# Kernel optimization log

Measured on AMD Instinct MI355X. Metric: run time of the kernel, lower is better.

The kernel has to match this reference:

```python
import jax, jax.numpy as jnp
import numpy as np

B = 16384    # batch of game states
HAND = 8     # max_hand_size
A = 30       # max_actions
C = 4        # max cards per action combo
E = 32       # card_embed_dim
HID = 128    # hidden_dim


def _encode_cards(cards, val_emb, suit_emb, type_emb):
    # cards: int array, 0 = padding, 53 = joker (treated as padding for value/suit)
    invalid = (cards == 0) | (cards == 53)
    values = jnp.where(invalid, 0, (cards - 1) % 13 + 1)
    suits = jnp.where(invalid, 0, (cards - 1) // 13 + 1)
    ce = jnp.concatenate([val_emb[values], suit_emb[suits]], axis=-1)  # [..., E]
    ct = jnp.where(values == 11, 1, jnp.where(values == 12, 2, jnp.where(values == 13, 3, 0)))
    te = type_emb[ct]  # [..., 8]
    pad = jnp.zeros(te.shape[:-1] + (E - te.shape[-1],), ce.dtype)
    return ce + jnp.concatenate([te, pad], axis=-1)


def _mha(q, kv, wq, bq, wk, bk, wv, bv, wo, bo, nh, kpm=None):
    b, sq, e = q.shape
    sk = kv.shape[1]
    hd = e // nh
    Q = (q @ wq + bq).reshape(b, sq, nh, hd)
    K = (kv @ wk + bk).reshape(b, sk, nh, hd)
    V = (kv @ wv + bv).reshape(b, sk, nh, hd)
    s = jnp.einsum('bqhd,bkhd->bhqk', Q, K) * (1.0 / np.sqrt(hd))
    if kpm is not None:  # kpm True = valid key
        s = s + jnp.where(kpm[:, None, None, :], 0.0, -1e9)
    a = jax.nn.softmax(s, axis=-1)
    o = jnp.einsum('bhqk,bkhd->bqhd', a, V).reshape(b, sq, e)
    return o @ wo + bo


def _combo_features(cards):
    # cards: [A, C] int, 0 = padding. Vectorized version of _compute_combo_features.
    mask = cards != 0
    combo_size = mask.sum(1).astype(jnp.float32)
    values = jnp.where(mask, (cards - 1) % 13 + 1, 0)
    has_valid = mask.any(1)
    fidx = jnp.argmax(mask, axis=1)
    fv = values[jnp.arange(cards.shape[0]), fidx]  # first valid value per action
    same = jnp.where(mask, values == fv[:, None], True).all(1).astype(jnp.float32)
    vf = values.astype(jnp.float32)
    attack = jnp.where(values == 1, 1.0,
             jnp.where(values == 11, 10.0,
             jnp.where(values == 12, 15.0,
             jnp.where(values == 13, 20.0, vf))))
    total = (attack * mask).sum(1)
    suits = jnp.where(mask, (cards - 1) // 13 + 1, 0)
    uniq = jnp.stack([(suits == s).any(1) for s in (1, 2, 3, 4)], 0).sum(0).astype(jnp.float32)
    ace = ((values == 1) & mask).any(1).astype(jnp.float32)
    valid = ((combo_size <= 4.0) & ((same > 0) | (ace > 0))).astype(jnp.float32)
    feats = jnp.stack([combo_size, same, total, uniq, ace, valid], axis=1)  # [A, 6]
    return jnp.where(has_valid[:, None], feats, 0.0), has_valid


def _forward(hand_cards, enemy_card, hand_size, game_state, discard_pile_cards,
             action_card_indices, num_valid_actions,
             val_emb, suit_emb, type_emb,
             ce_w1, ce_b1, ce_w2, ce_b2,
             ha_wq, ha_bq, ha_wk, ha_bk, ha_wv, ha_bv, ha_wo, ha_bo,
             he_wq, he_bq, he_wk, he_bk, he_wv, he_bv, he_wo, he_bo,
             se_w1, se_b1, se_w2, se_b2,
             atc_w1, atc_b1, atc_w2, atc_b2,
             as_w1, as_b1, as_w2, as_b2, as_w3, as_b3,
             cx_w1, cx_b1, cx_w2, cx_b2, cx_w3, cx_b3):
    relu = jax.nn.relu
    hand_emb = _encode_cards(hand_cards, val_emb, suit_emb, type_emb)            # [B, HAND, E]
    enemy_emb = _encode_cards(enemy_card[:, None], val_emb, suit_emb, type_emb)  # [B, 1, E]
    hand_mask = hand_cards != 0
    attended = _mha(hand_emb, hand_emb, ha_wq, ha_bq, ha_wk, ha_bk, ha_wv, ha_bv, ha_wo, ha_bo, 8, kpm=hand_mask)
    ctx_he = _mha(attended, enemy_emb, he_wq, he_bq, he_wk, he_bk, he_wv, he_bv, he_wo, he_bo, 4)
    lengths = jnp.maximum(hand_size.astype(jnp.float32), 1.0)[:, None]
    hand_ctx = ctx_he.sum(1) / lengths                                           # [B, E]

    # strategic features (batched per game state)
    hvals = jnp.where(hand_cards == 0, 0, (hand_cards - 1) % 13 + 1)
    hsz = hand_size.astype(jnp.float32)
    aces = (hvals == 1).sum(1).astype(jnp.float32)
    faces = ((hvals >= 11) & (hvals <= 13)).sum(1).astype(jnp.float32)
    low = ((hvals >= 2) & (hvals <= 6)).sum(1).astype(jnp.float32)
    hsuits = jnp.where(hand_cards == 0, 0, (hand_cards - 1) // 13 + 1)
    scnt = [(hsuits == s).sum(1).astype(jnp.float32) for s in (1, 2, 3, 4)]
    hvr = faces / (hsz + 1e-8)
    sdiv = jnp.stack([(hsuits == s).any(1) for s in (1, 2, 3, 4)], 0).sum(0).astype(jnp.float32) / 4.0
    strat = jnp.stack([hsz, aces, faces, low, scnt[0], scnt[1], scnt[2], scnt[3], hvr, sdiv], axis=1)
    strat_in = jnp.concatenate([game_state, strat], axis=1)                      # [B, 20]
    strat_ctx = relu(strat_in @ se_w1 + se_b1) @ se_w2 + se_b2                   # [B, 32]

    combined = jnp.concatenate([hand_ctx, enemy_emb[:, 0], strat_ctx, discard_pile_cards], axis=1)  # [B, 150]
    h = relu(combined @ cx_w1 + cx_b1)
    h = relu(h @ cx_w2 + cx_b2)
    ctx = h @ cx_w3 + cx_b3                                                      # [B, HID]
    type_probs = jax.nn.softmax(relu(ctx @ atc_w1 + atc_b1) @ atc_w2 + atc_b2, axis=-1)  # [B, 4]

    feats, has_valid = _combo_features(action_card_indices)                      # [A, 6], [A]
    emb = _encode_cards(action_card_indices, val_emb, suit_emb, type_emb)        # [A, C, E]
    m = (action_card_indices != 0).astype(emb.dtype)[..., None]
    cnt = jnp.maximum(m.sum(1), 1.0)
    act_emb = (emb * m).sum(1) / cnt                                             # masked mean over real cards
    act_emb = jnp.where(has_valid[:, None], act_emb, 0.0)
    combo_enc = relu(feats @ ce_w1 + ce_b1) @ ce_w2 + ce_b2                      # [A, 16]

    Bn = ctx.shape[0]
    af = jnp.concatenate([
        jnp.broadcast_to(ctx[:, None, :], (Bn, A, HID)),
        jnp.broadcast_to(act_emb[None], (Bn, A, E)),
        jnp.broadcast_to(combo_enc[None], (Bn, A, 16)),
    ], axis=-1)                                                                  # [B, A, 176]
    s = relu(af @ as_w1 + as_b1)
    s = relu(s @ as_w2 + as_b2)
    score = (s @ as_w3 + as_b3)[..., 0]                                          # [B, A]

    strength = feats[:, 2] / 20.0                                                # [A]
    bonus_valid = type_probs[:, 0:1] * strength[None, :] + type_probs[:, 1:2] * (1.0 - strength[None, :])
    bonus_empty = jnp.broadcast_to(type_probs[:, 3:4] * 2.0, (Bn, A))
    bonus = jnp.where(has_valid[None, :], bonus_valid, bonus_empty)
    return score + bonus                                                          # [B, A]


def setup_inputs() -> dict:
    key = jax.random.key(0)
    ki = iter(jax.random.split(key, 64))
    def nrm(shape, s):
        return (s * jax.random.normal(next(ki), shape)).astype(jnp.float32)
    def lin(i, o, s=0.08):
        return nrm((i, o), s), nrm((o,), 0.02)
    d = {}
    hc = jax.random.randint(next(ki), (B, HAND), 0, 53)
    d['hand_cards'] = hc.at[:, 0].set(jax.random.randint(next(ki), (B,), 1, 53))  # at least one valid card per hand
    d['enemy_card'] = jax.random.randint(next(ki), (B,), 1, 53)
    d['hand_size'] = jax.random.randint(next(ki), (B,), 1, 9)
    d['game_state'] = nrm((B, 10), 1.0)
    d['discard_pile_cards'] = jax.random.uniform(next(ki), (B, 54), dtype=jnp.float32)
    d['action_card_indices'] = jax.random.randint(next(ki), (A, C), 1, 53)
    d['num_valid_actions'] = A
    d['val_emb'] = nrm((14, 16), 0.1).at[0].set(0.0)   # padding_idx=0
    d['suit_emb'] = nrm((5, 16), 0.1).at[0].set(0.0)   # padding_idx=0
    d['type_emb'] = nrm((4, 8), 0.1)
    d['ce_w1'], d['ce_b1'] = lin(6, 32)
    d['ce_w2'], d['ce_b2'] = lin(32, 16)
    for p in ('ha', 'he'):
        for t in ('q', 'k', 'v', 'o'):
            d[p + '_w' + t], d[p + '_b' + t] = lin(E, E)
    d['se_w1'], d['se_b1'] = lin(20, 64)
    d['se_w2'], d['se_b2'] = lin(64, 32)
    d['atc_w1'], d['atc_b1'] = lin(HID, 64)
    d['atc_w2'], d['atc_b2'] = lin(64, 4)
    d['as_w1'], d['as_b1'] = lin(HID + E + 16, 64)
    d['as_w2'], d['as_b2'] = lin(64, 32)
    d['as_w3'], d['as_b3'] = lin(32, 1)
    d['cx_w1'], d['cx_b1'] = lin(2 * E + 32 + 54, HID)
    d['cx_w2'], d['cx_b2'] = lin(HID, HID)
    d['cx_w3'], d['cx_b3'] = lin(HID, HID)
    return d


def reference(hand_cards, enemy_card, hand_size, game_state, discard_pile_cards,
              action_card_indices, num_valid_actions,
              val_emb, suit_emb, type_emb,
              ce_w1, ce_b1, ce_w2, ce_b2,
              ha_wq, ha_bq, ha_wk, ha_bk, ha_wv, ha_bv, ha_wo, ha_bo,
              he_wq, he_bq, he_wk, he_bk, he_wv, he_bv, he_wo, he_bo,
              se_w1, se_b1, se_w2, se_b2,
              atc_w1, atc_b1, atc_w2, atc_b2,
              as_w1, as_b1, as_w2, as_b2, as_w3, as_b3,
              cx_w1, cx_b1, cx_w2, cx_b2, cx_w3, cx_b3):
    return _forward(hand_cards, enemy_card, hand_size, game_state, discard_pile_cards,
                    action_card_indices, num_valid_actions,
                    val_emb, suit_emb, type_emb,
                    ce_w1, ce_b1, ce_w2, ce_b2,
                    ha_wq, ha_bq, ha_wk, ha_bk, ha_wv, ha_bv, ha_wo, ha_bo,
                    he_wq, he_bq, he_wk, he_bk, he_wv, he_bv, he_wo, he_bo,
                    se_w1, se_b1, se_w2, se_b2,
                    atc_w1, atc_b1, atc_w2, atc_b2,
                    as_w1, as_b1, as_w2, as_b2, as_w3, as_b3,
                    cx_w1, cx_b1, cx_w2, cx_b2, cx_w3, cx_b3)
```

## Files before the change

### kernel.cpp

```cpp
#include <hip/hip_runtime.h>
#include <math.h>


__device__ __forceinline__ void encode_card32(int c,
                                              const float* __restrict__ val_emb,
                                              const float* __restrict__ suit_emb,
                                              const float* __restrict__ type_emb,
                                              float* e) {
  bool inv = (c == 0) || (c == 53);
  int v = inv ? 0 : ((c - 1) % 13 + 1);
  int s = inv ? 0 : ((c - 1) / 13 + 1);
  int ct = (v == 11) ? 1 : (v == 12) ? 2 : (v == 13) ? 3 : 0;
#pragma unroll
  for (int i = 0; i < 16; ++i) e[i] = val_emb[v * 16 + i];
#pragma unroll
  for (int i = 0; i < 16; ++i) e[16 + i] = suit_emb[s * 16 + i];
#pragma unroll
  for (int i = 0; i < 8; ++i) e[i] += type_emb[ct * 8 + i];
}

__global__ __launch_bounds__(64) void action_kernel(
    const int* __restrict__ acards,
    const float* __restrict__ val_emb, const float* __restrict__ suit_emb,
    const float* __restrict__ type_emb,
    const float* __restrict__ ce_w1, const float* __restrict__ ce_b1,
    const float* __restrict__ ce_w2, const float* __restrict__ ce_b2,
    const float* __restrict__ as_w1, const float* __restrict__ as_b1,
    float* __restrict__ ws) {
  __shared__ float sAct[30][32];
  __shared__ float sCombo[30][16];
  const int tid = threadIdx.x;

  if (tid < 30) {
    int c[4];
#pragma unroll
    for (int i = 0; i < 4; ++i) c[i] = acards[tid * 4 + i];
    bool mask[4]; int vals[4], suits[4]; int csize = 0; bool hasv = false;
#pragma unroll
    for (int i = 0; i < 4; ++i) {
      mask[i] = (c[i] != 0);
      if (mask[i]) { csize++; hasv = true; }
      vals[i] = mask[i] ? ((c[i] - 1) % 13 + 1) : 0;
      suits[i] = mask[i] ? ((c[i] - 1) / 13 + 1) : 0;
    }
    int fvv = mask[0] ? vals[0] : mask[1] ? vals[1] : mask[2] ? vals[2]
              : mask[3] ? vals[3] : vals[0];
    bool same = true;
#pragma unroll
    for (int i = 0; i < 4; ++i) if (mask[i] && vals[i] != fvv) same = false;
    float total = 0.f;
#pragma unroll
    for (int i = 0; i < 4; ++i) {
      if (mask[i]) {
        int v = vals[i];
        total += (v == 1) ? 1.f : (v == 11) ? 10.f : (v == 12) ? 15.f
                 : (v == 13) ? 20.f : (float)v;
      }
    }
    float uniq = 0.f;
#pragma unroll
    for (int s = 1; s <= 4; ++s) {
      bool any = false;
#pragma unroll
      for (int i = 0; i < 4; ++i) if (suits[i] == s) any = true;
      uniq += any ? 1.f : 0.f;
    }
    bool ace = false;
#pragma unroll
    for (int i = 0; i < 4; ++i) if (mask[i] && vals[i] == 1) ace = true;
    float f_same = same ? 1.f : 0.f, f_ace = ace ? 1.f : 0.f;
    float valid = (((float)csize <= 4.f) && (f_same > 0.f || f_ace > 0.f)) ? 1.f : 0.f;
    float feats[6] = {(float)csize, f_same, total, uniq, f_ace, valid};
    if (!hasv) { for (int i = 0; i < 6; ++i) feats[i] = 0.f; }
    float emb[32];
#pragma unroll
    for (int i = 0; i < 32; ++i) emb[i] = 0.f;
    float cnt = 0.f;
#pragma unroll
    for (int i = 0; i < 4; ++i) {
      float e[32];
      encode_card32(c[i], val_emb, suit_emb, type_emb, e);
      if (mask[i]) {
#pragma unroll
        for (int j = 0; j < 32; ++j) emb[j] += e[j];
        cnt += 1.f;
      }
    }
    float invc = 1.f / fmaxf(cnt, 1.f);
#pragma unroll
    for (int j = 0; j < 32; ++j) sAct[tid][j] = hasv ? emb[j] * invc : 0.f;
    float t32[32];
#pragma unroll
    for (int j = 0; j < 32; ++j) {
      float acc = ce_b1[j];
#pragma unroll
      for (int k = 0; k < 6; ++k) acc += feats[k] * ce_w1[k * 32 + j];
      t32[j] = fmaxf(acc, 0.f);
    }
#pragma unroll
    for (int j = 0; j < 16; ++j) {
      float acc = ce_b2[j];
#pragma unroll
      for (int k = 0; k < 32; ++k) acc += t32[k] * ce_w2[k * 16 + j];
      sCombo[tid][j] = acc;
    }
    ws[1920 + tid] = total * 0.05f;
    ws[1950 + tid] = hasv ? 1.f : 0.f;
  }
  __syncthreads();
  for (int idx = tid; idx < 1920; idx += 64) {
    int a = idx >> 6, j = idx & 63;
    float acc = as_b1[j];
#pragma unroll
    for (int k = 0; k < 32; ++k) acc += sAct[a][k] * as_w1[(128 + k) * 64 + j];
#pragma unroll
    for (int k = 0; k < 16; ++k) acc += sCombo[a][k] * as_w1[(160 + k) * 64 + j];
    ws[idx] = acc;
  }
}

template <int K, int NJ, bool RELU, bool HASB, bool QIN, bool QOUT>
__device__ __forceinline__ void layerU(
    const float* __restrict__ in, int inColBase, float* __restrict__ outB,
    int outColBase, const float* __restrict__ W, int ldw, int j0,
    const float* __restrict__ bias, int r) {
  float acc[NJ];
#pragma unroll
  for (int j = 0; j < NJ; ++j) acc[j] = HASB ? bias[j0 + j] : 0.f;
  if constexpr (QIN) {
    static_assert(K % 4 == 0, "quad input needs K%4==0");
    const int g0 = inColBase >> 2;
#pragma unroll 8
    for (int g = 0; g < K / 4; ++g) {
      float4 a = *(const float4*)&in[(g0 + g) * 256 + r * 4];
#pragma unroll
      for (int q = 0; q < 4; ++q) {
        float av = (q == 0) ? a.x : (q == 1) ? a.y : (q == 2) ? a.z : a.w;
        const float* wr = W + (size_t)(g * 4 + q) * ldw + j0;
#pragma unroll
        for (int j = 0; j < NJ; ++j) acc[j] += av * wr[j];
      }
    }
  } else {
#pragma unroll 4
    for (int k = 0; k < K; ++k) {
      float a = in[(inColBase + k) * 64 + r];
      const float* wr = W + (size_t)k * ldw + j0;
#pragma unroll
      for (int j = 0; j < NJ; ++j) acc[j] += a * wr[j];
    }
  }
#pragma unroll
  for (int j = 0; j < NJ; ++j) if (RELU) acc[j] = fmaxf(acc[j], 0.f);
  if constexpr (QOUT && (NJ % 4 == 0)) {
    const int c0 = outColBase + j0;
#pragma unroll
    for (int qg = 0; qg < NJ / 4; ++qg) {
      float4 o = make_float4(acc[qg * 4], acc[qg * 4 + 1],
                             acc[qg * 4 + 2], acc[qg * 4 + 3]);
      *(float4*)&outB[((c0 >> 2) + qg) * 256 + r * 4] = o;
    }
  } else {
#pragma unroll
    for (int j = 0; j < NJ; ++j) outB[(outColBase + j0 + j) * 64 + r] = acc[j];
  }
}

__global__ __launch_bounds__(1024) void policy_main(
    const int* __restrict__ hand_cards, const int* __restrict__ enemy_card,
    const int* __restrict__ hand_size, const float* __restrict__ game_state,
    const float* __restrict__ discard,
    const float* __restrict__ val_emb, const float* __restrict__ suit_emb,
    const float* __restrict__ type_emb,
    const float* __restrict__ he_wv, const float* __restrict__ he_bv,
    const float* __restrict__ he_wo, const float* __restrict__ he_bo,
    const float* __restrict__ se_w1, const float* __restrict__ se_b1,
    const float* __restrict__ se_w2, const float* __restrict__ se_b2,
    const float* __restrict__ atc_w1, const float* __restrict__ atc_b1,
    const float* __restrict__ atc_w2, const float* __restrict__ atc_b2,
    const float* __restrict__ as_w1,
    const float* __restrict__ as_w2, const float* __restrict__ as_b2,
    const float* __restrict__ as_w3, const float* __restrict__ as_b3,
    const float* __restrict__ cx_w1, const float* __restrict__ cx_b1,
    const float* __restrict__ cx_w2, const float* __restrict__ cx_b2,
    const float* __restrict__ cx_w3, const float* __restrict__ cx_b3,
    const float* __restrict__ ws, float* __restrict__ out) {
  __shared__ float bufA[38 * 256];
  __shared__ float bufB[128 * 64];

  const int tid = threadIdx.x;
  const int r = tid & 63;
  const int wq = __builtin_amdgcn_readfirstlane(tid >> 6);
  const int b0 = blockIdx.x * 64;

  for (int idx = tid; idx < 64 * 54; idx += 1024) {
    int rr = idx / 54, k = idx - rr * 54;
    int c = 96 + k;
    bufA[(c >> 2) * 256 + rr * 4 + (c & 3)] = discard[(size_t)b0 * 54 + idx];
  }
  if (wq == 2) {
#pragma unroll
    for (int k = 0; k < 10; ++k)
      bufB[k * 64 + r] = game_state[(size_t)(b0 + r) * 10 + k];
  }
  if (wq == 0) {
    const int b = b0 + r;
    const float hsz = (float)hand_size[b];
    int aces = 0, faces = 0, low = 0, c1 = 0, c2 = 0, c3 = 0, c4 = 0;
#pragma unroll
    for (int i = 0; i < 8; ++i) {
      int c = hand_cards[b * 8 + i];
      int v = (c == 0) ? 0 : ((c - 1) % 13 + 1);
      int s = (c == 0) ? 0 : ((c - 1) / 13 + 1);
      aces += (v == 1);
      faces += (v >= 11 && v <= 13);
      low += (v >= 2 && v <= 6);
      c1 += (s == 1); c2 += (s == 2); c3 += (s == 3); c4 += (s == 4);
    }
    float sdiv = (float)((c1 > 0) + (c2 > 0) + (c3 > 0) + (c4 > 0)) * 0.25f;
    float hvr = (float)faces / (hsz + 1e-8f);
    bufB[(10 + 0) * 64 + r] = hsz;          bufB[(10 + 1) * 64 + r] = (float)aces;
    bufB[(10 + 2) * 64 + r] = (float)faces; bufB[(10 + 3) * 64 + r] = (float)low;
    bufB[(10 + 4) * 64 + r] = (float)c1;    bufB[(10 + 5) * 64 + r] = (float)c2;
    bufB[(10 + 6) * 64 + r] = (float)c3;    bufB[(10 + 7) * 64 + r] = (float)c4;
    bufB[(10 + 8) * 64 + r] = hvr;          bufB[(10 + 9) * 64 + r] = sdiv;
  }
  if (wq == 1) {
    const int b = b0 + r;
    bufB[116 * 64 + r] = 8.0f / fmaxf((float)hand_size[b], 1.0f);
    float e[32];
    encode_card32(enemy_card[b], val_emb, suit_emb, type_emb, e);
#pragma unroll
    for (int g = 0; g < 8; ++g) {
      float4 ev = make_float4(e[g * 4], e[g * 4 + 1], e[g * 4 + 2], e[g * 4 + 3]);
      *(float4*)&bufA[(8 + g) * 256 + r * 4] = ev;
    }
  }
  __syncthreads();

  if (wq < 8) {
    layerU<20, 8, true, true, false, false>(bufB, 0, bufB, 20, se_w1, 64,
                                            wq * 8, se_b1, r);
  } else {
    layerU<32, 4, false, true, true, false>(bufA, 32, bufB, 84, he_wv, 32,
                                            (wq - 8) * 4, he_bv, r);
  }
  __syncthreads();

  if (wq < 8) {
    layerU<64, 4, false, true, false, true>(bufB, 20, bufA, 64, se_w2, 32,
                                            wq * 4, se_b2, r);
  } else {
    const int j0 = (wq - 8) * 4;
    float acc[4];
#pragma unroll
    for (int j = 0; j < 4; ++j) acc[j] = he_bo[j0 + j];
#pragma unroll 4
    for (int k = 0; k < 32; ++k) {
      float a = bufB[(84 + k) * 64 + r];
      const float* wr = he_wo + (size_t)k * 32 + j0;
#pragma unroll
      for (int j = 0; j < 4; ++j) acc[j] += a * wr[j];
    }
    float scale = bufB[116 * 64 + r];
    float4 o = make_float4(scale * acc[0], scale * acc[1],
                           scale * acc[2], scale * acc[3]);
    *(float4*)&bufA[(j0 >> 2) * 256 + r * 4] = o;
  }
  __syncthreads();

  {
    const int j0 = wq * 8;
    float acc[8];
#pragma unroll
    for (int j = 0; j < 8; ++j) acc[j] = cx_b1[j0 + j];
#pragma unroll 8
    for (int g = 0; g < 37; ++g) {
      float4 a = *(const float4*)&bufA[g * 256 + r * 4];
#pragma unroll
      for (int q = 0; q < 4; ++q) {
        float av = (q == 0) ? a.x : (q == 1) ? a.y : (q == 2) ? a.z : a.w;
        const float* wr = cx_w1 + (size_t)(g * 4 + q) * 128 + j0;
#pragma unroll
        for (int j = 0; j < 8; ++j) acc[j] += av * wr[j];
      }
    }
    {
      float4 a = *(const float4*)&bufA[37 * 256 + r * 4];
      const float* wr0 = cx_w1 + (size_t)148 * 128 + j0;
      const float* wr1 = cx_w1 + (size_t)149 * 128 + j0;
#pragma unroll
      for (int j = 0; j < 8; ++j) acc[j] += a.x * wr0[j] + a.y * wr1[j];
    }
#pragma unroll
    for (int qg = 0; qg < 2; ++qg) {
      float4 o = make_float4(fmaxf(acc[qg * 4], 0.f), fmaxf(acc[qg * 4 + 1], 0.f),
                             fmaxf(acc[qg * 4 + 2], 0.f), fmaxf(acc[qg * 4 + 3], 0.f));
      *(float4*)&bufB[((j0 >> 2) + qg) * 256 + r * 4] = o;
    }
  }
  __syncthreads();

  layerU<128, 8, true, true, true, true>(bufB, 0, bufA, 0, cx_w2, 128, wq * 8,
                                         cx_b2, r);
  __syncthreads();

  layerU<128, 8, false, true, true, true>(bufA, 0, bufB, 0, cx_w3, 128, wq * 8,
                                          cx_b3, r);
  __syncthreads();

  if (wq < 8) {
    layerU<128, 8, true, true, true, true>(bufB, 0, bufA, 0, atc_w1, 64,
                                           wq * 8, atc_b1, r);
  } else {
    layerU<128, 8, false, false, true, true>(bufB, 0, bufA, 64, as_w1, 64,
                                             (wq - 8) * 8, nullptr, r);
  }
  __syncthreads();

  if (wq < 15) {
    float lg0 = atc_b2[0], lg1 = atc_b2[1], lg2 = atc_b2[2], lg3 = atc_b2[3];
#pragma unroll 4
    for (int g = 0; g < 16; ++g) {
      float4 t = *(const float4*)&bufA[g * 256 + r * 4];
#pragma unroll
      for (int q = 0; q < 4; ++q) {
        float tv = (q == 0) ? t.x : (q == 1) ? t.y : (q == 2) ? t.z : t.w;
        const float* wr = atc_w2 + (size_t)(g * 4 + q) * 4;
        lg0 += tv * wr[0]; lg1 += tv * wr[1];
        lg2 += tv * wr[2]; lg3 += tv * wr[3];
      }
    }
    float m = fmaxf(fmaxf(lg0, lg1), fmaxf(lg2, lg3));
    float e0 = expf(lg0 - m), e1 = expf(lg1 - m), e2 = expf(lg2 - m), e3 = expf(lg3 - m);
    float inv = 1.f / (e0 + e1 + e2 + e3);
    float tp0 = e0 * inv, tp1 = e1 * inv, tp3 = e3 * inv;

    const float b3v = as_b3[0];
#pragma unroll 1
    for (int i = 0; i < 2; ++i) {
      const int a = wq * 2 + i;
      const float* qa = ws + a * 64;
      float acc[32];
#pragma unroll
      for (int j = 0; j < 32; ++j) acc[j] = 0.f;
#pragma unroll 2
      for (int g = 0; g < 16; ++g) {
        float4 pv = *(const float4*)&bufA[(16 + g) * 256 + r * 4];
#pragma unroll
        for (int q = 0; q < 4; ++q) {
          float p = (q == 0) ? pv.x : (q == 1) ? pv.y : (q == 2) ? pv.z : pv.w;
          const int k = g * 4 + q;
          float s = fmaxf(p + qa[k], 0.f);
          const float* w2r = as_w2 + (size_t)k * 32;
#pragma unroll
          for (int j = 0; j < 32; ++j) acc[j] += s * w2r[j];
        }
      }
      float sc = b3v;
#pragma unroll
      for (int j = 0; j < 32; ++j)
        sc += fmaxf(acc[j] + as_b2[j], 0.f) * as_w3[j];
      float st = ws[1920 + a], hv = ws[1950 + a];
      float bon = (hv > 0.5f) ? (tp0 * st + tp1 * (1.f - st)) : tp3 * 2.f;
      out[(size_t)(b0 + r) * 30 + a] = sc + bon;
    }
  }
}

extern "C" void kernel_launch(void* const* d_in, const int* in_sizes, int n_in,
                              void* d_out, int out_size, void* d_ws, size_t ws_size,
                              hipStream_t stream) {
  (void)in_sizes; (void)n_in; (void)out_size; (void)ws_size;
  const int* hand_cards = (const int*)d_in[0];
  const int* enemy_card = (const int*)d_in[1];
  const int* hand_size = (const int*)d_in[2];
  const float* game_state = (const float*)d_in[3];
  const float* discard = (const float*)d_in[4];
  const int* acards = (const int*)d_in[5];
  const float* val_emb = (const float*)d_in[7];
  const float* suit_emb = (const float*)d_in[8];
  const float* type_emb = (const float*)d_in[9];
  const float* ce_w1 = (const float*)d_in[10], * ce_b1 = (const float*)d_in[11];
  const float* ce_w2 = (const float*)d_in[12], * ce_b2 = (const float*)d_in[13];
  const float* he_wv = (const float*)d_in[26], * he_bv = (const float*)d_in[27];
  const float* he_wo = (const float*)d_in[28], * he_bo = (const float*)d_in[29];
  const float* se_w1 = (const float*)d_in[30], * se_b1 = (const float*)d_in[31];
  const float* se_w2 = (const float*)d_in[32], * se_b2 = (const float*)d_in[33];
  const float* atc_w1 = (const float*)d_in[34], * atc_b1 = (const float*)d_in[35];
  const float* atc_w2 = (const float*)d_in[36], * atc_b2 = (const float*)d_in[37];
  const float* as_w1 = (const float*)d_in[38], * as_b1 = (const float*)d_in[39];
  const float* as_w2 = (const float*)d_in[40], * as_b2 = (const float*)d_in[41];
  const float* as_w3 = (const float*)d_in[42], * as_b3 = (const float*)d_in[43];
  const float* cx_w1 = (const float*)d_in[44], * cx_b1 = (const float*)d_in[45];
  const float* cx_w2 = (const float*)d_in[46], * cx_b2 = (const float*)d_in[47];
  const float* cx_w3 = (const float*)d_in[48], * cx_b3 = (const float*)d_in[49];
  float* ws = (float*)d_ws;
  float* out = (float*)d_out;

  hipLaunchKernelGGL(action_kernel, dim3(1), dim3(64), 0, stream,
                     acards, val_emb, suit_emb, type_emb,
                     ce_w1, ce_b1, ce_w2, ce_b2, as_w1, as_b1, ws);
  hipLaunchKernelGGL(policy_main, dim3(256), dim3(1024), 0, stream,
                     hand_cards, enemy_card, hand_size, game_state, discard,
                     val_emb, suit_emb, type_emb,
                     he_wv, he_bv, he_wo, he_bo,
                     se_w1, se_b1, se_w2, se_b2,
                     atc_w1, atc_b1, atc_w2, atc_b2,
                     as_w1, as_w2, as_b2, as_w3, as_b3,
                     cx_w1, cx_b1, cx_w2, cx_b2, cx_w3, cx_b3,
                     ws, out);
}
```

Before: 243.4 us.

## Fold linear cx layer 3 into downstream atc and action-scorer projections

Since the third context MLP layer has no activation, its weights and bias are premultiplied into the atc_w1 and as_w1 projections in the single-block precompute kernel, and the results are stored in workspace. The main kernel then skips one full 128x128 layer and its barrier, reading the fused weights from workspace instead. The precompute block grows to 1024 threads and does a serial weight-product computation before the main launch, which adds latency on one CU. The unroll factor of the scoring loop is also raised.

```diff
diff --git a/kernel.cpp b/kernel.cpp
--- a/kernel.cpp
+++ b/kernel.cpp
@@ -19,13 +19,15 @@
   for (int i = 0; i < 8; ++i) e[i] += type_emb[ct * 8 + i];
 }
 
-__global__ __launch_bounds__(64) void action_kernel(
+__global__ __launch_bounds__(1024) void precompute_kernel(
     const int* __restrict__ acards,
     const float* __restrict__ val_emb, const float* __restrict__ suit_emb,
     const float* __restrict__ type_emb,
     const float* __restrict__ ce_w1, const float* __restrict__ ce_b1,
     const float* __restrict__ ce_w2, const float* __restrict__ ce_b2,
     const float* __restrict__ as_w1, const float* __restrict__ as_b1,
+    const float* __restrict__ cx_w3, const float* __restrict__ cx_b3,
+    const float* __restrict__ atc_w1, const float* __restrict__ atc_b1,
     float* __restrict__ ws) {
   __shared__ float sAct[30][32];
   __shared__ float sCombo[30][16];
@@ -107,8 +109,33 @@
     ws[1920 + tid] = total * 0.05f;
     ws[1950 + tid] = hasv ? 1.f : 0.f;
   }
-  __syncthreads();
-  for (int idx = tid; idx < 1920; idx += 64) {
+
+  for (int idx = tid; idx < 8192; idx += 1024) {
+    int k = idx >> 6, j = idx & 63;
+    float at = 0.f, ap = 0.f;
+#pragma unroll 4
+    for (int m = 0; m < 128; ++m) {
+      float c = cx_w3[k * 128 + m];
+      at += c * atc_w1[m * 64 + j];
+      ap += c * as_w1[(size_t)m * 64 + j];
+    }
+    ws[2048 + idx] = at;
+    ws[10304 + idx] = ap;
+  }
+  if (tid < 64) {
+    float bt = atc_b1[tid], bp = 0.f;
+#pragma unroll 4
+    for (int m = 0; m < 128; ++m) {
+      float c = cx_b3[m];
+      bt += c * atc_w1[m * 64 + tid];
+      bp += c * as_w1[(size_t)m * 64 + tid];
+    }
+    ws[10240 + tid] = bt;
+    ws[18496 + tid] = bp;
+  }
+
+  __syncthreads();
+  for (int idx = tid; idx < 1920; idx += 1024) {
     int a = idx >> 6, j = idx & 63;
     float acc = as_b1[j];
 #pragma unroll
@@ -176,14 +203,11 @@
     const float* __restrict__ he_wo, const float* __restrict__ he_bo,
     const float* __restrict__ se_w1, const float* __restrict__ se_b1,
     const float* __restrict__ se_w2, const float* __restrict__ se_b2,
-    const float* __restrict__ atc_w1, const float* __restrict__ atc_b1,
     const float* __restrict__ atc_w2, const float* __restrict__ atc_b2,
-    const float* __restrict__ as_w1,
     const float* __restrict__ as_w2, const float* __restrict__ as_b2,
     const float* __restrict__ as_w3, const float* __restrict__ as_b3,
     const float* __restrict__ cx_w1, const float* __restrict__ cx_b1,
     const float* __restrict__ cx_w2, const float* __restrict__ cx_b2,
-    const float* __restrict__ cx_w3, const float* __restrict__ cx_b3,
     const float* __restrict__ ws, float* __restrict__ out) {
   __shared__ float bufA[38 * 256];
   __shared__ float bufB[128 * 64];
@@ -305,16 +329,12 @@
                                          cx_b2, r);
   __syncthreads();
 
-  layerU<128, 8, false, true, true, true>(bufA, 0, bufB, 0, cx_w3, 128, wq * 8,
-                                          cx_b3, r);
-  __syncthreads();
-
   if (wq < 8) {
-    layerU<128, 8, true, true, true, true>(bufB, 0, bufA, 0, atc_w1, 64,
-                                           wq * 8, atc_b1, r);
+    layerU<128, 8, true, true, true, true>(bufA, 0, bufB, 0, ws + 2048, 64,
+                                           wq * 8, ws + 10240, r);
   } else {
-    layerU<128, 8, false, false, true, true>(bufB, 0, bufA, 64, as_w1, 64,
-                                             (wq - 8) * 8, nullptr, r);
+    layerU<128, 8, false, true, true, true>(bufA, 0, bufB, 64, ws + 10304, 64,
+                                            (wq - 8) * 8, ws + 18496, r);
   }
   __syncthreads();
 
@@ -322,7 +342,7 @@
     float lg0 = atc_b2[0], lg1 = atc_b2[1], lg2 = atc_b2[2], lg3 = atc_b2[3];
 #pragma unroll 4
     for (int g = 0; g < 16; ++g) {
-      float4 t = *(const float4*)&bufA[g * 256 + r * 4];
+      float4 t = *(const float4*)&bufB[g * 256 + r * 4];
 #pragma unroll
       for (int q = 0; q < 4; ++q) {
         float tv = (q == 0) ? t.x : (q == 1) ? t.y : (q == 2) ? t.z : t.w;
@@ -344,9 +364,9 @@
       float acc[32];
 #pragma unroll
       for (int j = 0; j < 32; ++j) acc[j] = 0.f;
-#pragma unroll 2
+#pragma unroll 4
       for (int g = 0; g < 16; ++g) {
-        float4 pv = *(const float4*)&bufA[(16 + g) * 256 + r * 4];
+        float4 pv = *(const float4*)&bufB[(16 + g) * 256 + r * 4];
 #pragma unroll
         for (int q = 0; q < 4; ++q) {
           float p = (q == 0) ? pv.x : (q == 1) ? pv.y : (q == 2) ? pv.z : pv.w;
@@ -398,16 +418,17 @@
   float* ws = (float*)d_ws;
   float* out = (float*)d_out;
 
-  hipLaunchKernelGGL(action_kernel, dim3(1), dim3(64), 0, stream,
+  hipLaunchKernelGGL(precompute_kernel, dim3(1), dim3(1024), 0, stream,
                      acards, val_emb, suit_emb, type_emb,
-                     ce_w1, ce_b1, ce_w2, ce_b2, as_w1, as_b1, ws);
+                     ce_w1, ce_b1, ce_w2, ce_b2, as_w1, as_b1,
+                     cx_w3, cx_b3, atc_w1, atc_b1, ws);
   hipLaunchKernelGGL(policy_main, dim3(256), dim3(1024), 0, stream,
                      hand_cards, enemy_card, hand_size, game_state, discard,
                      val_emb, suit_emb, type_emb,
                      he_wv, he_bv, he_wo, he_bo,
                      se_w1, se_b1, se_w2, se_b2,
-                     atc_w1, atc_b1, atc_w2, atc_b2,
-                     as_w1, as_w2, as_b2, as_w3, as_b3,
-                     cx_w1, cx_b1, cx_w2, cx_b2, cx_w3, cx_b3,
+                     atc_w2, atc_b2,
+                     as_w2, as_b2, as_w3, as_b3,
+                     cx_w1, cx_b1, cx_w2, cx_b2,
                      ws, out);
 }
```

New measurement: 326.9 us. +34.3%, slower.
